# Performance work log

Hardware: AMD Instinct MI355X
Metric: run time of the kernel (lower is better)

The kernel has to match this reference:

```python
import jax, jax.numpy as jnp
import numpy as np

B, C, L = 2, 2048, 8192  # batch, channels = d_model*(order-1), seq_len


def setup_inputs() -> dict:
    key = jax.random.key(0)
    k1, k2, k3 = jax.random.split(key, 3)
    x = jax.random.normal(k1, (B, C, L), dtype=jnp.float32)
    # implicit long-conv filter produced by HyenaFilter, materialized as a learned tensor
    k = jax.random.normal(k2, (C, L), dtype=jnp.float32) * 0.02
    bias = jax.random.normal(k3, (C,), dtype=jnp.float32)
    return {"x": x, "k": k, "bias": bias}


def reference(x, k, bias):
    # FFT-based causal depthwise long convolution (Hyena fftconv):
    #   y[b,c,t] = sum_{s<=t} k[c,s] * x[b,c,t-s]  + bias[c] * x[b,c,t]
    L_ = x.shape[-1]
    fft_size = 2 * L_  # zero-pad to 2L for linear (non-circular) convolution
    k_f = jnp.fft.rfft(k, n=fft_size) / fft_size          # [C, fft/2+1] complex
    x_f = jnp.fft.rfft(x, n=fft_size)                     # [B, C, fft/2+1]
    y = jnp.fft.irfft(x_f * k_f, n=fft_size, norm="forward")[..., :L_]
    return y + x * bias[None, :, None]
```

## Files before the change

kernel.cpp:

```cpp
#include <hip/hip_runtime.h>

#define LSEQ 8192
#define NFFT 8192
#define NT2 512
#define CCH 2048
#define TWO_PI 6.283185307179586f
#define PI_F  3.14159265358979323846f
#define KSTRIDE 8208

__device__ __forceinline__ int SL2(int i) { return i ^ (((i >> 4) & 15) << 1); }

__device__ __forceinline__ float2 cmul(float2 a, float2 b) {
    return b * a.x + make_float2(-b.y, b.x) * a.y;
}
__device__ __forceinline__ float2 conjf2(float2 a) { return make_float2(a.x, -a.y); }

template<int SGN>
__device__ __forceinline__ float2 muli(float2 t) {
    return (SGN < 0) ? make_float2(t.y, -t.x) : make_float2(-t.y, t.x);
}

template<int SGN>
__device__ __forceinline__ void dft4(float2& a0, float2& a1, float2& a2, float2& a3) {
    float2 t0 = a0 + a2, t1 = a0 - a2, t2 = a1 + a3, t3 = a1 - a3;
    float2 u = muli<SGN>(t3);
    a0 = t0 + t2; a1 = t1 + u; a2 = t0 - t2; a3 = t1 - u;
}

template<int SGN>
__device__ __forceinline__ void dft8(float2& v0, float2& v1, float2& v2, float2& v3,
                                     float2& v4, float2& v5, float2& v6, float2& v7) {
    float2 e0 = v0, e1 = v2, e2 = v4, e3 = v6;
    float2 o0 = v1, o1 = v3, o2 = v5, o3 = v7;
    dft4<SGN>(e0, e1, e2, e3);
    dft4<SGN>(o0, o1, o2, o3);
    const float sg = (float)SGN;
    const float H = 0.7071067811865476f;
    float2 t1 = cmul(o1, make_float2( H, sg * H));
    float2 t2 = muli<SGN>(o2);
    float2 t3 = cmul(o3, make_float2(-H, sg * H));
    v0 = e0 + o0; v4 = e0 - o0;
    v1 = e1 + t1; v5 = e1 - t1;
    v2 = e2 + t2; v6 = e2 - t2;
    v3 = e3 + t3; v7 = e3 - t3;
}

__device__ __forceinline__ void rdr(const float2* p, float2& lo, float2& hi) {
    const float4 v = *reinterpret_cast<const float4*>(p);
    lo = make_float2(v.x, v.y);
    hi = make_float2(v.z, v.w);
}
__device__ __forceinline__ void wrr(float2* p, float2 lo, float2 hi) {
    *reinterpret_cast<float4*>(p) = make_float4(lo.x, lo.y, hi.x, hi.y);
}
__device__ __forceinline__ void wrp(float2* ds, int e, float2 lo, float2 hi) {
    wrr(&ds[SL2(e)], lo, hi);
}

#define RD8X                                                                  \
    float2 a0,a1,a2,a3,a4,a5,a6,a7,b0,b1,b2,b3,b4,b5,b6,b7;                   \
    {   const float2* p_ = ds + SL2(B_);                                      \
        rdr(p_,        a0, b0);                                               \
        rdr(p_ + 1024, a1, b1);                                               \
        rdr(p_ + 2048, a2, b2);                                               \
        rdr(p_ + 3072, a3, b3);                                               \
        rdr(p_ + 4096, a4, b4);                                               \
        rdr(p_ + 5120, a5, b5);                                               \
        rdr(p_ + 6144, a6, b6);                                               \
        rdr(p_ + 7168, a7, b7);                                               \
    }

#define DFT8AB(SGN)                                                           \
    dft8<(SGN)>(a0,a1,a2,a3,a4,a5,a6,a7);                                     \
    dft8<(SGN)>(b0,b1,b2,b3,b4,b5,b6,b7);

#define TWID(SGN, NSv, WDC, WDS) {                                            \
    float s_, c_;                                                             \
    __sincosf((float)(SGN) * TWO_PI / (float)((NSv) * 8) *                    \
              (float)(B_ & ((NSv) - 1)), &s_, &c_);                           \
    const float2 w1a = make_float2(c_, s_);                                   \
    a1 = cmul(a1, w1a);                                                       \
    const float2 w2a = cmul(w1a, w1a);                                        \
    a2 = cmul(a2, w2a);                                                       \
    const float2 w3a = cmul(w2a, w1a);                                        \
    a3 = cmul(a3, w3a);                                                       \
    const float2 w4a = cmul(w2a, w2a);                                        \
    a4 = cmul(a4, w4a);                                                       \
    a5 = cmul(a5, cmul(w3a, w2a));                                            \
    a6 = cmul(a6, cmul(w3a, w3a));                                            \
    a7 = cmul(a7, cmul(w4a, w3a));                                            \
    const float2 w1b = cmul(w1a, make_float2((WDC), (float)(SGN) * (WDS)));   \
    b1 = cmul(b1, w1b);                                                       \
    const float2 w2b = cmul(w1b, w1b);                                        \
    b2 = cmul(b2, w2b);                                                       \
    const float2 w3b = cmul(w2b, w1b);                                        \
    b3 = cmul(b3, w3b);                                                       \
    const float2 w4b = cmul(w2b, w2b);                                        \
    b4 = cmul(b4, w4b);                                                       \
    b5 = cmul(b5, cmul(w3b, w2b));                                            \
    b6 = cmul(b6, cmul(w3b, w3b));                                            \
    b7 = cmul(b7, cmul(w4b, w3b));                                            \
}

#define WR8P(NSv) {                                                           \
    const int i_ = B_ & ((NSv) - 1);                                          \
    const int d_ = ((B_ - i_) << 3) + i_;                                     \
    wrp(ds, d_,             a0, b0);                                          \
    wrp(ds, d_ +     (NSv), a1, b1);                                          \
    wrp(ds, d_ + 2 * (NSv), a2, b2);                                          \
    wrp(ds, d_ + 3 * (NSv), a3, b3);                                          \
    wrp(ds, d_ + 4 * (NSv), a4, b4);                                          \
    wrp(ds, d_ + 5 * (NSv), a5, b5);                                          \
    wrp(ds, d_ + 6 * (NSv), a6, b6);                                          \
    wrp(ds, d_ + 7 * (NSv), a7, b7);                                          \
}

#define WR8SEQ {                                                              \
    const int d_ = B_ << 3;                                                   \
    wrp(ds, d_,      a0, a1);                                                 \
    wrp(ds, d_ +  2, a2, a3);                                                 \
    wrp(ds, d_ +  4, a4, a5);                                                 \
    wrp(ds, d_ +  6, a6, a7);                                                 \
    wrp(ds, d_ +  8, b0, b1);                                                 \
    wrp(ds, d_ + 10, b2, b3);                                                 \
    wrp(ds, d_ + 12, b4, b5);                                                 \
    wrp(ds, d_ + 14, b6, b7);                                                 \
}

#define P8MID(SGN, NSv, WDC, WDS) {                                           \
    RD8X                                                                      \
    TWID(SGN, NSv, WDC, WDS)                                                  \
    DFT8AB(SGN)                                                               \
    __syncthreads();                                                          \
    WR8P(NSv)                                                                 \
    __syncthreads();                                                          \
}

#define WD8C   0.9951847266721969f
#define WD8S   0.0980171403295606f
#define WD64C  0.9999247018391445f
#define WD64S  0.012271538285719925f
#define WD16C  0.9987954562051724f
#define WD16S  0.049067674327418015f
#define WD128C 0.9999811752826011f
#define WD128S 0.006135884649154475f
#define WDF_C  0.9999997058628822f
#define WDF_S  0.0007669903187427045f

#define DFT16M(SGN, P) {                                                            \
    dft4<(SGN)>(P##0, P##4, P##8,  P##12);                                          \
    dft4<(SGN)>(P##1, P##5, P##9,  P##13);                                          \
    dft4<(SGN)>(P##2, P##6, P##10, P##14);                                          \
    dft4<(SGN)>(P##3, P##7, P##11, P##15);                                          \
    const float sg_ = (float)(SGN);                                                 \
    const float2 tw1_ = make_float2( 0.9238795325112867f,  sg_ * 0.3826834323650898f); \
    const float2 tw2_ = make_float2( 0.7071067811865476f,  sg_ * 0.7071067811865476f); \
    const float2 tw3_ = make_float2( 0.3826834323650898f,  sg_ * 0.9238795325112867f); \
    const float2 tw6_ = make_float2(-0.7071067811865476f,  sg_ * 0.7071067811865476f); \
    const float2 tw9_ = make_float2(-0.9238795325112867f, -sg_ * 0.3826834323650898f); \
    P##5  = cmul(P##5,  tw1_);                                                      \
    P##6  = cmul(P##6,  tw2_);                                                      \
    P##7  = cmul(P##7,  tw3_);                                                      \
    P##9  = cmul(P##9,  tw2_);                                                      \
    P##10 = muli<(SGN)>(P##10);                                                     \
    P##11 = cmul(P##11, tw6_);                                                      \
    P##13 = cmul(P##13, tw3_);                                                      \
    P##14 = cmul(P##14, tw6_);                                                      \
    P##15 = cmul(P##15, tw9_);                                                      \
    dft4<(SGN)>(P##0,  P##1,  P##2,  P##3);                                         \
    dft4<(SGN)>(P##4,  P##5,  P##6,  P##7);                                         \
    dft4<(SGN)>(P##8,  P##9,  P##10, P##11);                                        \
    dft4<(SGN)>(P##12, P##13, P##14, P##15);                                        \
}

#define R16_LOAD_TWIDDLE(SGN)                                                 \
    float2 m0,m1,m2,m3,m4,m5,m6,m7,m8,m9,m10,m11,m12,m13,m14,m15;             \
    {   const float2* p_ = ds + SL2(tid);                                     \
        m0  = p_[0];    m1  = p_[512];  m2  = p_[1024]; m3  = p_[1536];       \
        m4  = p_[2048]; m5  = p_[2560]; m6  = p_[3072]; m7  = p_[3584];       \
        m8  = p_[4096]; m9  = p_[4608]; m10 = p_[5120]; m11 = p_[5632];       \
        m12 = p_[6144]; m13 = p_[6656]; m14 = p_[7168]; m15 = p_[7680];       \
    }                                                                         \
    {   float s_, c_;                                                         \
        __sincosf((float)(SGN) * TWO_PI / 8192.0f * (float)tid, &s_, &c_);    \
        const float2 w1 = make_float2(c_, s_);                                \
        m1 = cmul(m1, w1);                                                    \
        const float2 w2 = cmul(w1, w1);   m2  = cmul(m2,  w2);                \
        const float2 w3 = cmul(w2, w1);   m3  = cmul(m3,  w3);                \
        const float2 w4 = cmul(w2, w2);   m4  = cmul(m4,  w4);                \
        const float2 w5 = cmul(w3, w2);   m5  = cmul(m5,  w5);                \
        const float2 w6 = cmul(w3, w3);   m6  = cmul(m6,  w6);                \
        const float2 w7 = cmul(w4, w3);   m7  = cmul(m7,  w7);                \
        const float2 w8 = cmul(w4, w4);   m8  = cmul(m8,  w8);                \
        m9  = cmul(m9,  cmul(w5, w4));                                        \
        m10 = cmul(m10, cmul(w5, w5));                                        \
        m11 = cmul(m11, cmul(w6, w5));                                        \
        m12 = cmul(m12, cmul(w6, w6));                                        \
        m13 = cmul(m13, cmul(w7, w6));                                        \
        m14 = cmul(m14, cmul(w7, w7));                                        \
        m15 = cmul(m15, cmul(w8, w7));                                        \
    }

#define R16_STORE_LDS {                                                       \
    float2* p_ = ds + SL2(tid);                                               \
    p_[0]    = m0;  p_[512]  = m4;  p_[1024] = m8;  p_[1536] = m12;           \
    p_[2048] = m1;  p_[2560] = m5;  p_[3072] = m9;  p_[3584] = m13;           \
    p_[4096] = m2;  p_[4608] = m6;  p_[5120] = m10; p_[5632] = m14;           \
    p_[6144] = m3;  p_[6656] = m7;  p_[7168] = m11; p_[7680] = m15;           \
}

#define UE1 make_float2(0.9807852804032304f, 0.1950903220161283f)

#define UNT(R, MW, VOUT) {                                                    \
    float2 Wm_ = ds[mb_ - 512 * (R)];                                         \
    float2 E_ = (MW + conjf2(Wm_)) * 0.5f;                                    \
    float2 D_ = (MW - conjf2(Wm_)) * 0.5f;                                    \
    float2 O_ = make_float2(D_.y, -D_.x);                                     \
    float2 Xj_ = E_ + cmul(O_, conjf2(cs));                                   \
    float2 Xm_ = conjf2(E_) - cmul(conjf2(O_), cs);                           \
    float2 Zj_ = cmul(Xj_, kc[tid + 512 * (R)]);                              \
    float2 Zm_ = cmul(Xm_, kc[8192 - tid - 512 * (R)]);                       \
    float2 P_ = Zj_ + conjf2(Zm_);                                            \
    float2 Q_ = Zj_ - conjf2(Zm_);                                            \
    VOUT = P_ + cmul(Q_, make_float2(-cs.y, cs.x));                           \
    cs = cmul(cs, UE1);                                                       \
}

__global__ __launch_bounds__(NT2)
void hyena_kfft8(const float* __restrict__ k, const float* __restrict__ bias,
                 float2* __restrict__ kw)
{
    __shared__ alignas(16) float2 ds[NFFT];
    const int c = blockIdx.x, tid = threadIdx.x;
    const int B_ = tid << 1;
    const float* kp = k + (size_t)c * LSEQ;
    const float bsv = bias[c];

    {
        float2 a0,a1,a2,a3,a4,a5,a6,a7,b0,b1,b2,b3,b4,b5,b6,b7;
        float4 v;
        v = *(const float4*)&kp[(B_ << 1)];
        a0 = make_float2(v.x, v.y); b0 = make_float2(v.z, v.w);
        if (tid == 0) a0.x += bsv;
        v = *(const float4*)&kp[(B_ << 1) + 2048];
        a1 = make_float2(v.x, v.y); b1 = make_float2(v.z, v.w);
        v = *(const float4*)&kp[(B_ << 1) + 4096];
        a2 = make_float2(v.x, v.y); b2 = make_float2(v.z, v.w);
        v = *(const float4*)&kp[(B_ << 1) + 6144];
        a3 = make_float2(v.x, v.y); b3 = make_float2(v.z, v.w);
        a4 = a5 = a6 = a7 = b4 = b5 = b6 = b7 = make_float2(0.f, 0.f);
        DFT8AB(-1)
        WR8SEQ
        __syncthreads();
    }
    P8MID(-1, 8,  WD8C,  WD8S)
    P8MID(-1, 64, WD64C, WD64S)
    {
        R16_LOAD_TWIDDLE(-1)
        DFT16M(-1, m)
        R16_STORE_LDS
    }
    __syncthreads();

    {
        const float sc = 1.0f / 16384.0f;
        float2* kc = kw + (size_t)c * KSTRIDE;
        float2* pj_ = ds + SL2(tid);
        const int mb_ = (tid == 0) ? 8192 : (7680 + SL2(512 - tid));
        float s0_, c0_;
        __sincosf(PI_F / 8192.0f * (float)tid, &s0_, &c0_);
        float2 cs = make_float2(c0_, s0_);
#pragma unroll
        for (int r = 0; r < 8; r++) {
            if (tid == 0 && r == 0) {
                float2 W0 = ds[SL2(0)];
                kc[0]    = make_float2((W0.x + W0.y) * sc, 0.f);
                kc[8192] = make_float2((W0.x - W0.y) * sc, 0.f);
                float2 W4 = ds[SL2(4096)];
                kc[4096] = make_float2(W4.x * sc, -W4.y * sc);
            } else {
                const int j  = tid + (r << 9);
                const int jm = NFFT - j;
                float2 Wj = pj_[r << 9];
                float2 Wm = ds[mb_ - (r << 9)];
                float2 E = (Wj + conjf2(Wm)) * 0.5f;
                float2 D = (Wj - conjf2(Wm)) * 0.5f;
                float2 O = make_float2(D.y, -D.x);
                const float c_ = cs.x, s_ = cs.y;
                float2 tO = cmul(O, make_float2(c_, -s_));
                float2 uO = cmul(conjf2(O), make_float2(c_, s_));
                kc[j]  = (E + tO) * sc;
                kc[jm] = (conjf2(E) - uO) * sc;
            }
            cs = cmul(cs, UE1);
        }
    }
}

__global__ __launch_bounds__(NT2)
void hyena_xconv8(const float* __restrict__ x, const float2* __restrict__ kw,
                  float* __restrict__ y)
{
    __shared__ alignas(16) float2 ds[NFFT];
    const int bid = blockIdx.x, tid = threadIdx.x;
    const int c = bid >> 1, b = bid & 1;
    const int B_ = tid << 1;
    const float* xp = x + ((size_t)(b * CCH + c)) * LSEQ;
    float*       yp = y + ((size_t)(b * CCH + c)) * LSEQ;

    {
        float2 a0,a1,a2,a3,a4,a5,a6,a7,b0,b1,b2,b3,b4,b5,b6,b7;
        float4 v;
        v = *(const float4*)&xp[(B_ << 1)];
        a0 = make_float2(v.x, v.y); b0 = make_float2(v.z, v.w);
        v = *(const float4*)&xp[(B_ << 1) + 2048];
        a1 = make_float2(v.x, v.y); b1 = make_float2(v.z, v.w);
        v = *(const float4*)&xp[(B_ << 1) + 4096];
        a2 = make_float2(v.x, v.y); b2 = make_float2(v.z, v.w);
        v = *(const float4*)&xp[(B_ << 1) + 6144];
        a3 = make_float2(v.x, v.y); b3 = make_float2(v.z, v.w);
        a4 = a5 = a6 = a7 = b4 = b5 = b6 = b7 = make_float2(0.f, 0.f);
        DFT8AB(-1)
        WR8SEQ
        __syncthreads();
    }
    P8MID(-1, 8,  WD8C,  WD8S)
    P8MID(-1, 64, WD64C, WD64S)

    {
        R16_LOAD_TWIDDLE(-1)
        DFT16M(-1, m)
        R16_STORE_LDS
        __syncthreads();

        const float2* kc = kw + (size_t)c * KSTRIDE;
        const int mb_ = (tid == 0) ? 8192 : (7680 + SL2(512 - tid));
        float s0_, c0_;
        __sincosf(PI_F / 8192.0f * (float)tid, &s0_, &c0_);
        float2 cs = make_float2(c0_, s0_);
        float2 v0,v1,v2,v3,v4,v5,v6,v7,v8,v9,v10,v11,v12,v13,v14,v15;

        if (tid == 0) {
            float X0 = m0.x + m0.y, XN = m0.x - m0.y;
            float2 K0 = kc[0], KN = kc[8192];
            float2 Z0 = K0 * X0;
            float2 ZN = KN * XN;
            v0 = make_float2(Z0.x + ZN.x - (Z0.y - ZN.y),
                             Z0.y + ZN.y + (Z0.x - ZN.x));
            cs = cmul(cs, UE1);
        } else {
            UNT(0, m0, v0)
        }
        UNT(1,  m4,  v1)
        UNT(2,  m8,  v2)
        UNT(3,  m12, v3)
        UNT(4,  m1,  v4)
        UNT(5,  m5,  v5)
        UNT(6,  m9,  v6)
        UNT(7,  m13, v7)
        UNT(8,  m2,  v8)
        UNT(9,  m6,  v9)
        UNT(10, m10, v10)
        UNT(11, m14, v11)
        UNT(12, m3,  v12)
        UNT(13, m7,  v13)
        UNT(14, m11, v14)
        UNT(15, m15, v15)
        __syncthreads();

        DFT16M(1, v)
        const int d0_ = tid << 4;
        wrp(ds, d0_,      v0,  v4);
        wrp(ds, d0_ +  2, v8,  v12);
        wrp(ds, d0_ +  4, v1,  v5);
        wrp(ds, d0_ +  6, v9,  v13);
        wrp(ds, d0_ +  8, v2,  v6);
        wrp(ds, d0_ + 10, v10, v14);
        wrp(ds, d0_ + 12, v3,  v7);
        wrp(ds, d0_ + 14, v11, v15);
        __syncthreads();
    }

    P8MID(1, 16,  WD16C,  WD16S)
    P8MID(1, 128, WD128C, WD128S)

    {
        RD8X
        TWID(1, 1024, WDF_C, WDF_S)
        DFT8AB(1)
        *(float4*)&yp[(B_) << 1]        = make_float4(a0.x, a0.y, b0.x, b0.y);
        *(float4*)&yp[(B_ + 1024) << 1] = make_float4(a1.x, a1.y, b1.x, b1.y);
        *(float4*)&yp[(B_ + 2048) << 1] = make_float4(a2.x, a2.y, b2.x, b2.y);
        *(float4*)&yp[(B_ + 3072) << 1] = make_float4(a3.x, a3.y, b3.x, b3.y);
    }
}

extern "C" void kernel_launch(void* const* d_in, const int* in_sizes, int n_in,
                              void* d_out, int out_size, void* d_ws, size_t ws_size,
                              hipStream_t stream) {
    const float* x    = (const float*)d_in[0];
    const float* k    = (const float*)d_in[1];
    const float* bias = (const float*)d_in[2];
    float* y          = (float*)d_out;
    float2* kw        = (float2*)d_ws;

    hyena_kfft8 <<<dim3(CCH),     dim3(NT2), 0, stream>>>(k, bias, kw);
    hyena_xconv8<<<dim3(2 * CCH), dim3(NT2), 0, stream>>>(x, kw, y);
}
```

Measured before the change: 193.7 us.

## Exploit conjugate symmetry to halve LDS stores and untangle work in FFT conv

The forward FFT's last stage now stores only the upper half of outputs to LDS, and each thread processes symmetric pairs (j, N-j) together: the k-kernel writes both bins per pair, and the x-kernel computes both the j and mirrored outputs, writing the mirror back into LDS. This halves the untangle loop count and the LDS traffic. The final inverse radix-8 stage computes only the four outputs actually stored (the first L samples). An extra __syncthreads is added, and the in-place LDS writeback relies on a careful index/ownership argument.

```diff
diff --git a/kernel.cpp b/kernel.cpp
--- a/kernel.cpp
+++ b/kernel.cpp
@@ -43,6 +43,21 @@
     v1 = e1 + t1; v5 = e1 - t1;
     v2 = e2 + t2; v6 = e2 - t2;
     v3 = e3 + t3; v7 = e3 - t3;
+}
+
+template<int SGN>
+__device__ __forceinline__ void dft8_lo(float2& v0, float2& v1, float2& v2, float2& v3,
+                                        float2 v4, float2 v5, float2 v6, float2 v7) {
+    float2 e0 = v0, e1 = v2, e2 = v4, e3 = v6;
+    float2 o0 = v1, o1 = v3, o2 = v5, o3 = v7;
+    dft4<SGN>(e0, e1, e2, e3);
+    dft4<SGN>(o0, o1, o2, o3);
+    const float sg = (float)SGN;
+    const float H = 0.7071067811865476f;
+    float2 t1 = cmul(o1, make_float2( H, sg * H));
+    float2 t2 = muli<SGN>(o2);
+    float2 t3 = cmul(o3, make_float2(-H, sg * H));
+    v0 = e0 + o0; v1 = e1 + t1; v2 = e2 + t2; v3 = e3 + t3;
 }
 
 __device__ __forceinline__ void rdr(const float2* p, float2& lo, float2& hi) {
@@ -201,17 +216,15 @@
         m15 = cmul(m15, cmul(w8, w7));                                        \
     }
 
-#define R16_STORE_LDS {                                                       \
+#define R16_STORE_HI {                                                        \
     float2* p_ = ds + SL2(tid);                                               \
-    p_[0]    = m0;  p_[512]  = m4;  p_[1024] = m8;  p_[1536] = m12;           \
-    p_[2048] = m1;  p_[2560] = m5;  p_[3072] = m9;  p_[3584] = m13;           \
     p_[4096] = m2;  p_[4608] = m6;  p_[5120] = m10; p_[5632] = m14;           \
     p_[6144] = m3;  p_[6656] = m7;  p_[7168] = m11; p_[7680] = m15;           \
 }
 
 #define UE1 make_float2(0.9807852804032304f, 0.1950903220161283f)
 
-#define UNT(R, MW, VOUT) {                                                    \
+#define PAIR(R, MW, VOUT) {                                                   \
     float2 Wm_ = ds[mb_ - 512 * (R)];                                         \
     float2 E_ = (MW + conjf2(Wm_)) * 0.5f;                                    \
     float2 D_ = (MW - conjf2(Wm_)) * 0.5f;                                    \
@@ -223,7 +236,9 @@
     float2 P_ = Zj_ + conjf2(Zm_);                                            \
     float2 Q_ = Zj_ - conjf2(Zm_);                                            \
     VOUT = P_ + cmul(Q_, make_float2(-cs.y, cs.x));                           \
-    cs = cmul(cs, UE1);                                                       \
+    float2 P2_ = Zm_ + conjf2(Zj_);                                           \
+    float2 Q2_ = Zm_ - conjf2(Zj_);                                           \
+    ds[mb_ - 512 * (R)] = P2_ + cmul(Q2_, make_float2(-cs.y, -cs.x));         \
 }
 
 __global__ __launch_bounds__(NT2)
@@ -255,45 +270,43 @@
     }
     P8MID(-1, 8,  WD8C,  WD8S)
     P8MID(-1, 64, WD64C, WD64S)
-    {
-        R16_LOAD_TWIDDLE(-1)
-        DFT16M(-1, m)
-        R16_STORE_LDS
-    }
+
+    R16_LOAD_TWIDDLE(-1)
+    DFT16M(-1, m)
+    R16_STORE_HI
     __syncthreads();
 
     {
         const float sc = 1.0f / 16384.0f;
         float2* kc = kw + (size_t)c * KSTRIDE;
-        float2* pj_ = ds + SL2(tid);
         const int mb_ = (tid == 0) ? 8192 : (7680 + SL2(512 - tid));
         float s0_, c0_;
         __sincosf(PI_F / 8192.0f * (float)tid, &s0_, &c0_);
         float2 cs = make_float2(c0_, s0_);
-#pragma unroll
-        for (int r = 0; r < 8; r++) {
-            if (tid == 0 && r == 0) {
-                float2 W0 = ds[SL2(0)];
-                kc[0]    = make_float2((W0.x + W0.y) * sc, 0.f);
-                kc[8192] = make_float2((W0.x - W0.y) * sc, 0.f);
-                float2 W4 = ds[SL2(4096)];
-                kc[4096] = make_float2(W4.x * sc, -W4.y * sc);
-            } else {
-                const int j  = tid + (r << 9);
-                const int jm = NFFT - j;
-                float2 Wj = pj_[r << 9];
-                float2 Wm = ds[mb_ - (r << 9)];
-                float2 E = (Wj + conjf2(Wm)) * 0.5f;
-                float2 D = (Wj - conjf2(Wm)) * 0.5f;
-                float2 O = make_float2(D.y, -D.x);
-                const float c_ = cs.x, s_ = cs.y;
-                float2 tO = cmul(O, make_float2(c_, -s_));
-                float2 uO = cmul(conjf2(O), make_float2(c_, s_));
-                kc[j]  = (E + tO) * sc;
-                kc[jm] = (conjf2(E) - uO) * sc;
-            }
-            cs = cmul(cs, UE1);
+#define KPAIR(R, MW) {                                                        \
+        float2 Wm_ = ds[mb_ - 512 * (R)];                                     \
+        float2 E_ = (MW + conjf2(Wm_)) * 0.5f;                                \
+        float2 D_ = (MW - conjf2(Wm_)) * 0.5f;                                \
+        float2 O_ = make_float2(D_.y, -D_.x);                                 \
+        kc[tid + 512 * (R)]        = (E_ + cmul(O_, conjf2(cs))) * sc;        \
+        kc[8192 - tid - 512 * (R)] = (conjf2(E_) - cmul(conjf2(O_), cs)) * sc;\
+    }
+        if (tid == 0) {
+            kc[0]    = make_float2((m0.x + m0.y) * sc, 0.f);
+            kc[8192] = make_float2((m0.x - m0.y) * sc, 0.f);
+            kc[4096] = make_float2(m2.x * sc, -m2.y * sc);
+        } else {
+            KPAIR(0, m0)
         }
+        cs = cmul(cs, UE1);
+        KPAIR(1, m4)  cs = cmul(cs, UE1);
+        KPAIR(2, m8)  cs = cmul(cs, UE1);
+        KPAIR(3, m12) cs = cmul(cs, UE1);
+        KPAIR(4, m1)  cs = cmul(cs, UE1);
+        KPAIR(5, m5)  cs = cmul(cs, UE1);
+        KPAIR(6, m9)  cs = cmul(cs, UE1);
+        KPAIR(7, m13)
+#undef KPAIR
     }
 }
 
@@ -330,7 +343,7 @@
     {
         R16_LOAD_TWIDDLE(-1)
         DFT16M(-1, m)
-        R16_STORE_LDS
+        R16_STORE_HI
         __syncthreads();
 
         const float2* kc = kw + (size_t)c * KSTRIDE;
@@ -343,32 +356,32 @@
         if (tid == 0) {
             float X0 = m0.x + m0.y, XN = m0.x - m0.y;
             float2 K0 = kc[0], KN = kc[8192];
-            float2 Z0 = K0 * X0;
-            float2 ZN = KN * XN;
+            float2 Z0 = K0 * X0, ZN = KN * XN;
             v0 = make_float2(Z0.x + ZN.x - (Z0.y - ZN.y),
                              Z0.y + ZN.y + (Z0.x - ZN.x));
-            cs = cmul(cs, UE1);
+            float2 Z4 = cmul(conjf2(m2), kc[4096]);
+            v8 = make_float2(2.f * Z4.x, -2.f * Z4.y);
         } else {
-            UNT(0, m0, v0)
+            PAIR(0, m0, v0)
         }
-        UNT(1,  m4,  v1)
-        UNT(2,  m8,  v2)
-        UNT(3,  m12, v3)
-        UNT(4,  m1,  v4)
-        UNT(5,  m5,  v5)
-        UNT(6,  m9,  v6)
-        UNT(7,  m13, v7)
-        UNT(8,  m2,  v8)
-        UNT(9,  m6,  v9)
-        UNT(10, m10, v10)
-        UNT(11, m14, v11)
-        UNT(12, m3,  v12)
-        UNT(13, m7,  v13)
-        UNT(14, m11, v14)
-        UNT(15, m15, v15)
-        __syncthreads();
-
+        cs = cmul(cs, UE1);
+        PAIR(1, m4,  v1)  cs = cmul(cs, UE1);
+        PAIR(2, m8,  v2)  cs = cmul(cs, UE1);
+        PAIR(3, m12, v3)  cs = cmul(cs, UE1);
+        PAIR(4, m1,  v4)  cs = cmul(cs, UE1);
+        PAIR(5, m5,  v5)  cs = cmul(cs, UE1);
+        PAIR(6, m9,  v6)  cs = cmul(cs, UE1);
+        PAIR(7, m13, v7)
+        __syncthreads();
+
+        {
+            const float2* p_ = ds + SL2(tid);
+            if (tid != 0) v8 = p_[4096];
+            v9  = p_[4608]; v10 = p_[5120]; v11 = p_[5632];
+            v12 = p_[6144]; v13 = p_[6656]; v14 = p_[7168]; v15 = p_[7680];
+        }
         DFT16M(1, v)
+        __syncthreads();
         const int d0_ = tid << 4;
         wrp(ds, d0_,      v0,  v4);
         wrp(ds, d0_ +  2, v8,  v12);
@@ -387,7 +400,8 @@
     {
         RD8X
         TWID(1, 1024, WDF_C, WDF_S)
-        DFT8AB(1)
+        dft8_lo<1>(a0, a1, a2, a3, a4, a5, a6, a7);
+        dft8_lo<1>(b0, b1, b2, b3, b4, b5, b6, b7);
         *(float4*)&yp[(B_) << 1]        = make_float4(a0.x, a0.y, b0.x, b0.y);
         *(float4*)&yp[(B_ + 1024) << 1] = make_float4(a1.x, a1.y, b1.x, b1.y);
         *(float4*)&yp[(B_ + 2048) << 1] = make_float4(a2.x, a2.y, b2.x, b2.y);
```

After: 181.4 us. 1.07x faster.
